# Kernel optimization log

Hardware: AMD Instinct MI355X
Metric: run time of the kernel (lower is better)

Reference implementation:

```python
import jax, jax.numpy as jnp
import numpy as np

N = 50000      # nodes
E = 600000     # edges
C = 32         # in_features (channels)
COUT = 32      # out_features
NB = 8         # n_basis
NS = 10        # n_species
H = 64         # radial MLP hidden
NPATH = 5      # uvu paths for l_max=1: (0,0,0),(0,1,1),(1,0,1),(1,1,0),(1,1,1)
AVG = 12.0     # avg_n_neighbors
RS = 1.6765324703310907  # rescaled SiLU constant


def _rescaled_silu(x):
    return RS * jax.nn.silu(x)


def setup_inputs() -> dict:
    key = jax.random.key(0)
    ks = jax.random.split(key, 16)
    return {
        'node_attrs': jax.random.uniform(ks[0], (N, NS), dtype=jnp.float32),
        'node_feats': jax.random.normal(ks[1], (N, C, 4), dtype=jnp.float32),
        'edge_attrs': jax.random.normal(ks[2], (E, 1, 4), dtype=jnp.float32),
        'edge_feats': jax.random.normal(ks[3], (E, NB), dtype=jnp.float32),
        'W_first': jax.random.normal(ks[4], (2, C, C), dtype=jnp.float32),
        'Wr0': jax.random.normal(ks[5], (H, NB), dtype=jnp.float32),
        'Wr1': jax.random.normal(ks[6], (H, H), dtype=jnp.float32),
        'Wr2': jax.random.normal(ks[7], (H, H), dtype=jnp.float32),
        'Wr3': jax.random.normal(ks[8], (NPATH * C, H), dtype=jnp.float32),
        'W_second0': jax.random.normal(ks[9], (COUT, 2 * C), dtype=jnp.float32),
        'W_second1': jax.random.normal(ks[10], (COUT, 3 * C), dtype=jnp.float32),
        'W_skip': jax.random.normal(ks[11], (2, C, NS, C), dtype=jnp.float32),
        'idx_i': jnp.sort(jax.random.randint(ks[12], (E,), 0, N)),
        'idx_j': jax.random.randint(ks[13], (E,), 0, N),
    }


def reference(node_attrs, node_feats, edge_attrs, edge_feats, W_first, Wr0, Wr1,
              Wr2, Wr3, W_second0, W_second1, W_skip, idx_i, idx_j):
    # ---- skip_tp: uvw tensor product with l=0 node_attrs (species-dependent mixing per l)
    sc0 = jnp.einsum('ncm,nv,cvw->nwm', node_feats[:, :, :1], node_attrs, W_skip[0]) / np.sqrt(C * NS)
    sc1 = jnp.einsum('ncm,nv,cvw->nwm', node_feats[:, :, 1:4], node_attrs, W_skip[1]) / np.sqrt(C * NS)
    sc = jnp.concatenate([sc0, sc1], axis=-1)  # [N, C, 4]

    # ---- linear_first: per-l channel mixing
    x0 = jnp.einsum('ncm,dc->ndm', node_feats[:, :, :1], W_first[0]) / np.sqrt(C)   # [N,C,1]
    x1 = jnp.einsum('ncm,dc->ndm', node_feats[:, :, 1:4], W_first[1]) / np.sqrt(C)  # [N,C,3]

    # ---- radial MLP: Linear+RescaledSiLU chain, last SiLU dropped
    h = _rescaled_silu(edge_feats @ Wr0.T / np.sqrt(NB))
    h = _rescaled_silu(h @ Wr1.T / np.sqrt(H))
    h = _rescaled_silu(h @ Wr2.T / np.sqrt(H))
    w = (h @ Wr3.T / np.sqrt(H)).reshape(E, NPATH, C)  # per-edge, per-path, per-channel weights

    # ---- gather sender features
    xj0 = x0[idx_j][:, :, 0]   # [E, C]
    xj1 = x1[idx_j]            # [E, C, 3]
    y0 = edge_attrs[:, 0, 0]   # [E]      l=0 harmonic
    y1 = edge_attrs[:, 0, 1:4] # [E, 3]   l=1 harmonic

    # ---- uvu weighted tensor product (l_max=1 CG: scalar mult, dot, cross)
    p0 = w[:, 0] * xj0 * y0[:, None]                                   # (0,0,0) -> l=0
    p1 = w[:, 1, :, None] * xj0[:, :, None] * y1[:, None, :]          # (0,1,1) -> l=1
    p2 = w[:, 2, :, None] * xj1 * y0[:, None, None]                   # (1,0,1) -> l=1
    p3 = w[:, 3] * jnp.einsum('ecm,em->ec', xj1, y1)                  # (1,1,0) -> l=0
    p4 = w[:, 4, :, None] * jnp.cross(xj1, y1[:, None, :])            # (1,1,1) -> l=1

    # ---- scatter-add messages to receivers
    seg = lambda m: jax.ops.segment_sum(m, idx_i, num_segments=N)
    msg0 = seg(jnp.stack([p0, p3], axis=1))  # [N, 2, C]
    msg1 = seg(jnp.stack([p1, p2, p4], axis=1))  # [N, 3, C, 3]

    # ---- linear_second: mix (paths x channels) -> out_features per l
    out0 = jnp.einsum('npc,dpc->nd', msg0, W_second0.reshape(COUT, 2, C)) / np.sqrt(2 * C)
    out1 = jnp.einsum('npcm,dpc->ndm', msg1, W_second1.reshape(COUT, 3, C)) / np.sqrt(3 * C)
    message = jnp.concatenate([out0[:, :, None], out1], axis=-1) / AVG  # [N, COUT, 4]
    return message, sc
```

## Files before the change

kernel.cpp:

```cpp
#include <hip/hip_runtime.h>
#include <math.h>

#define N_NODES 50000
#define N_EDGES 600000

constexpr float RS          = 1.6765324703310907f;
constexpr float INV_SQRT8   = 0.35355339059327373f;
constexpr float INV8        = 0.125f;
constexpr float INV_SQRT320 = 0.05590169943749474f;
constexpr float INV_SQRT32  = 0.17677669529663687f;
constexpr float INV_SQRT96  = 0.10206207261596575f;
constexpr float INV_AVG     = 1.0f / 12.0f;

constexpr size_t OFF_X     = 0;
constexpr size_t OFF_ROW   = 25600000;
constexpr size_t OFF_FRAG  = 25800064;
constexpr size_t OFF_FRAG2 = 25841024;
constexpr size_t OFF_W     = 25931136;

typedef __attribute__((ext_vector_type(8))) short bfrag;
typedef __attribute__((ext_vector_type(4))) float ffrag;

__device__ __forceinline__ float rsilu(float z) {
  return RS * z / (1.0f + __expf(-z));
}
__device__ __forceinline__ unsigned short f2bf(float x) {
  unsigned u = __float_as_uint(x);
  u += 0x7FFFu + ((u >> 16) & 1u);
  return (unsigned short)(u >> 16);
}
__device__ __forceinline__ float bf2f(unsigned short u) {
  return __uint_as_float(((unsigned)u) << 16);
}

__global__ __launch_bounds__(256) void k_rowstart(const int* __restrict__ idx_i,
                                                  int* __restrict__ row,
                                                  int E, int N) {
  int e = blockIdx.x * 256 + threadIdx.x;
  if (e >= E) return;
  int cur  = idx_i[e];
  int prev = (e == 0) ? -1 : idx_i[e - 1];
  for (int n = prev + 1; n <= cur; ++n) row[n] = e;
  if (e == E - 1) {
    for (int n = cur + 1; n <= N; ++n) row[n] = E;
  }
}

__global__ __launch_bounds__(256) void k_prep(const float* __restrict__ Wr0,
                                              const float* __restrict__ Wr1,
                                              const float* __restrict__ Wr2,
                                              const float* __restrict__ Wr3,
                                              unsigned short* __restrict__ frag) {
  int t = blockIdx.x * 256 + threadIdx.x;
  int f    = t >> 9;
  int lane = (t >> 3) & 63;
  int j    = t & 7;
  int n16  = lane & 15, quad = lane >> 4;
  float v;
  if (f < 4) {
    int d = f * 16 + n16, k = quad * 8 + j;
    v = (k < 8) ? Wr0[d * 8 + k] : 0.f;
  } else if (f < 12) {
    int ff = f - 4, ntile = ff >> 1, ks = ff & 1;
    int d = ntile * 16 + n16, k = ks * 32 + quad * 8 + j;
    v = Wr1[d * 64 + k];
  } else if (f < 20) {
    int ff = f - 12, ntile = ff >> 1, ks = ff & 1;
    int d = ntile * 16 + n16, k = ks * 32 + quad * 8 + j;
    v = Wr2[d * 64 + k];
  } else {
    int ff = f - 20, ntile = ff >> 1, ks = ff & 1;
    int d = ntile * 16 + n16, k = ks * 32 + quad * 8 + j;
    v = Wr3[d * 64 + k];
  }
  frag[t] = f2bf(v);
}

__global__ __launch_bounds__(256) void k_prep2(const float* __restrict__ Wsk,
                                               const float* __restrict__ Wf,
                                               unsigned short* __restrict__ frag2) {
  int t = blockIdx.x * 256 + threadIdx.x;
  int f    = t >> 9;
  int lane = (t >> 3) & 63;
  int j    = t & 7;
  int n16  = lane & 15, quad = lane >> 4;
  int ks = f >> 3, nt = f & 7;
  int k   = ks * 32 + quad * 8 + j;
  int col = nt * 16 + n16;
  float v = 0.f;
  if (k < 320) {
    int vv = k >> 5, c = k & 31;
    if (col < 32)       v = Wsk[(c * 10 + vv) * 32 + col] * INV_SQRT320;
    else if (col < 64)  v = Wsk[((32 + c) * 10 + vv) * 32 + (col - 32)] * INV_SQRT320;
  } else {
    int c = k - 320;
    if (col >= 96)      v = Wf[1024 + (col - 96) * 32 + c] * INV_SQRT32;
    else if (col >= 64) v = Wf[(col - 64) * 32 + c] * INV_SQRT32;
  }
  frag2[t] = f2bf(v);
}

__global__ __launch_bounds__(256) void k_node_mfma(const float* __restrict__ attrs,
                                                   const float* __restrict__ feats,
                                                   const unsigned short* __restrict__ frag2,
                                                   float* __restrict__ out_sc,
                                                   float* __restrict__ x_ws) {
  int tid = threadIdx.x;
  int wave = tid >> 6, lane = tid & 63;
  int quad = lane >> 4, l16 = lane & 15;
  int nb = blockIdx.x * 32 + wave * 8;

  float featsF[2][8];
  float a[2][10];
#pragma unroll
  for (int mt = 0; mt < 2; ++mt) {
    int nodeA = nb + mt * 4 + (l16 >> 2);
    if (nodeA > N_NODES - 1) nodeA = N_NODES - 1;
    int m = l16 & 3;
#pragma unroll
    for (int j = 0; j < 8; ++j)
      featsF[mt][j] = feats[(size_t)nodeA * 128 + (quad * 8 + j) * 4 + m];
#pragma unroll
    for (int v = 0; v < 10; ++v) a[mt][v] = attrs[nodeA * 10 + v];
  }

  ffrag acc[2][8];
#pragma unroll
  for (int mt = 0; mt < 2; ++mt)
#pragma unroll
    for (int nt = 0; nt < 8; ++nt) acc[mt][nt] = (ffrag){0.f, 0.f, 0.f, 0.f};

#pragma unroll
  for (int ks = 0; ks < 11; ++ks) {
    bfrag Ab[2];
#pragma unroll
    for (int mt = 0; mt < 2; ++mt) {
      union { unsigned short s8[8]; bfrag v; } pk;
#pragma unroll
      for (int j = 0; j < 8; ++j) {
        float val = (ks < 10) ? a[mt][ks] * featsF[mt][j] : featsF[mt][j];
        pk.s8[j] = f2bf(val);
      }
      Ab[mt] = pk.v;
    }
#pragma unroll
    for (int nt = 0; nt < 8; ++nt) {
      bfrag B = *(const bfrag*)(frag2 + ((size_t)(ks * 8 + nt) * 64 + lane) * 8);
      acc[0][nt] = __builtin_amdgcn_mfma_f32_16x16x32_bf16(Ab[0], B, acc[0][nt], 0, 0, 0);
      acc[1][nt] = __builtin_amdgcn_mfma_f32_16x16x32_bf16(Ab[1], B, acc[1][nt], 0, 0, 0);
    }
  }

#pragma unroll
  for (int mt = 0; mt < 2; ++mt) {
    int node = nb + mt * 4 + quad;
    if (node < N_NODES) {
      float4 sc0 = {acc[mt][0][0], acc[mt][2][1], acc[mt][2][2], acc[mt][2][3]};
      float4 sc1 = {acc[mt][1][0], acc[mt][3][1], acc[mt][3][2], acc[mt][3][3]};
      float4 x0  = {acc[mt][4][0], acc[mt][6][1], acc[mt][6][2], acc[mt][6][3]};
      float4 x1  = {acc[mt][5][0], acc[mt][7][1], acc[mt][7][2], acc[mt][7][3]};
      ((float4*)out_sc)[(size_t)node * 32 + l16]      = sc0;
      ((float4*)out_sc)[(size_t)node * 32 + 16 + l16] = sc1;
      ((float4*)x_ws)[(size_t)node * 32 + l16]        = x0;
      ((float4*)x_ws)[(size_t)node * 32 + 16 + l16]   = x1;
    }
  }
}

#define MLP_M 128
__global__ __launch_bounds__(256) void k_mlp(const float* __restrict__ ef,
                                             const unsigned short* __restrict__ frag,
                                             unsigned short* __restrict__ w_out,
                                             int E) {
  __shared__ __align__(16) unsigned short H[4][32][168];
  int tid = threadIdx.x;
  int wave = tid >> 6, lane = tid & 63;
  int quad = lane >> 4, l16 = lane & 15;
  int m0 = blockIdx.x * MLP_M + wave * 32;
  unsigned short (*Hw)[168] = H[wave];

  bfrag a1[2];
#pragma unroll
  for (int mt = 0; mt < 2; ++mt) {
    float vals[8] = {0.f, 0.f, 0.f, 0.f, 0.f, 0.f, 0.f, 0.f};
    if (quad == 0) {
      int r = m0 + mt * 16 + l16;
      if (r > E - 1) r = E - 1;
      const float4* p = (const float4*)(ef + (size_t)r * 8);
      float4 u0 = p[0], u1 = p[1];
      vals[0] = u0.x; vals[1] = u0.y; vals[2] = u0.z; vals[3] = u0.w;
      vals[4] = u1.x; vals[5] = u1.y; vals[6] = u1.z; vals[7] = u1.w;
    }
    union { unsigned short s[8]; bfrag v; } pk;
#pragma unroll
    for (int j = 0; j < 8; ++j) pk.s[j] = f2bf(vals[j]);
    a1[mt] = pk.v;
  }
#pragma unroll
  for (int nt = 0; nt < 4; ++nt) {
    const bfrag* bp = (const bfrag*)(frag + ((size_t)(nt) * 64 + lane) * 8);
    bfrag b = *bp;
    ffrag acc0 = {0.f, 0.f, 0.f, 0.f}, acc1 = acc0;
    acc0 = __builtin_amdgcn_mfma_f32_16x16x32_bf16(a1[0], b, acc0, 0, 0, 0);
    acc1 = __builtin_amdgcn_mfma_f32_16x16x32_bf16(a1[1], b, acc1, 0, 0, 0);
#pragma unroll
    for (int r = 0; r < 4; ++r) {
      Hw[0 * 16 + quad * 4 + r][nt * 16 + l16] = f2bf(rsilu(acc0[r] * INV_SQRT8));
      Hw[1 * 16 + quad * 4 + r][nt * 16 + l16] = f2bf(rsilu(acc1[r] * INV_SQRT8));
    }
  }

  bfrag A[2][2];
#pragma unroll 1
  for (int L = 0; L < 2; ++L) {
    int fbase = 4 + L * 8;
#pragma unroll
    for (int mt = 0; mt < 2; ++mt)
#pragma unroll
      for (int ks = 0; ks < 2; ++ks)
        A[mt][ks] = *(const bfrag*)&Hw[mt * 16 + l16][ks * 32 + quad * 8];
#pragma unroll
    for (int nt = 0; nt < 4; ++nt) {
      ffrag acc0 = {0.f, 0.f, 0.f, 0.f}, acc1 = acc0;
#pragma unroll
      for (int ks = 0; ks < 2; ++ks) {
        bfrag b = *(const bfrag*)(frag + ((size_t)(fbase + nt * 2 + ks) * 64 + lane) * 8);
        acc0 = __builtin_amdgcn_mfma_f32_16x16x32_bf16(A[0][ks], b, acc0, 0, 0, 0);
        acc1 = __builtin_amdgcn_mfma_f32_16x16x32_bf16(A[1][ks], b, acc1, 0, 0, 0);
      }
#pragma unroll
      for (int r = 0; r < 4; ++r) {
        Hw[0 * 16 + quad * 4 + r][nt * 16 + l16] = f2bf(rsilu(acc0[r] * INV8));
        Hw[1 * 16 + quad * 4 + r][nt * 16 + l16] = f2bf(rsilu(acc1[r] * INV8));
      }
    }
  }

#pragma unroll
  for (int mt = 0; mt < 2; ++mt)
#pragma unroll
    for (int ks = 0; ks < 2; ++ks)
      A[mt][ks] = *(const bfrag*)&Hw[mt * 16 + l16][ks * 32 + quad * 8];
#pragma unroll 2
  for (int nt = 0; nt < 10; ++nt) {
    ffrag acc0 = {0.f, 0.f, 0.f, 0.f}, acc1 = acc0;
#pragma unroll
    for (int ks = 0; ks < 2; ++ks) {
      bfrag b = *(const bfrag*)(frag + ((size_t)(20 + nt * 2 + ks) * 64 + lane) * 8);
      acc0 = __builtin_amdgcn_mfma_f32_16x16x32_bf16(A[0][ks], b, acc0, 0, 0, 0);
      acc1 = __builtin_amdgcn_mfma_f32_16x16x32_bf16(A[1][ks], b, acc1, 0, 0, 0);
    }
#pragma unroll
    for (int r = 0; r < 4; ++r) {
      Hw[0 * 16 + quad * 4 + r][nt * 16 + l16] = f2bf(acc0[r] * INV8);
      Hw[1 * 16 + quad * 4 + r][nt * 16 + l16] = f2bf(acc1[r] * INV8);
    }
  }

#pragma unroll 2
  for (int it = 0; it < 10; ++it) {
    int c = it * 64 + lane;
    int row = c / 20, off = c % 20;
    int grow = m0 + row;
    uint4 v = *(const uint4*)&Hw[row][off * 8];
    if (grow < E)
      *(uint4*)(w_out + (size_t)grow * 160 + off * 8) = v;
  }
}

__global__ __launch_bounds__(256) void k_msg(const unsigned short* __restrict__ w_ws,
                                             const float* __restrict__ x_ws,
                                             const float* __restrict__ ea,
                                             const int* __restrict__ idx_j,
                                             const int* __restrict__ row,
                                             const float* __restrict__ Ws0,
                                             const float* __restrict__ Ws1,
                                             float* __restrict__ out_msg) {
  __shared__ float msg[8][353];
  __shared__ float W0T[64 * 33];
  __shared__ float W1T[96 * 33];

  int tid = threadIdx.x;
  for (int t = tid; t < 2048; t += 256) {
    int d = t >> 6, k = t & 63;
    W0T[k * 33 + d] = Ws0[t];
  }
  for (int t = tid; t < 3072; t += 256) {
    int d = t / 96, k = t % 96;
    W1T[k * 33 + d] = Ws1[t];
  }

  int ln = tid >> 5, c = tid & 31;
  int n = blockIdx.x * 8 + ln;
  int e0 = row[n], e1 = row[n + 1];

  float m00 = 0.f, m01 = 0.f;
  float m10x = 0.f, m10y = 0.f, m10z = 0.f;
  float m11x = 0.f, m11y = 0.f, m11z = 0.f;
  float m12x = 0.f, m12y = 0.f, m12z = 0.f;

  for (int base = e0; base < e1; base += 32) {
    int rem = e1 - base;
    int cnt = rem < 32 ? rem : 32;
    int jidx = base + (c < cnt ? c : cnt - 1);
    int j_c = __builtin_nontemporal_load(idx_j + jidx);

    for (int b = 0; b < cnt; b += 4) {
      int mvalid = cnt - b;
      float4 xj[4], y[4];
      float wv[4][5];
#pragma unroll
      for (int t = 0; t < 4; ++t) {
        int tt = (t < mvalid) ? t : 0;
        int e = base + b + tt;
        int j = __shfl(j_c, b + tt, 32);
        xj[t] = ((const float4*)x_ws)[(size_t)j * 32 + c];
        y[t]  = ((const float4*)ea)[e];
        const unsigned short* wr = w_ws + (size_t)e * 160;
        wv[t][0] = bf2f(__builtin_nontemporal_load(wr + c));
        wv[t][1] = bf2f(__builtin_nontemporal_load(wr + 32 + c));
        wv[t][2] = bf2f(__builtin_nontemporal_load(wr + 64 + c));
        wv[t][3] = bf2f(__builtin_nontemporal_load(wr + 96 + c));
        wv[t][4] = bf2f(__builtin_nontemporal_load(wr + 128 + c));
      }
#pragma unroll
      for (int t = 0; t < 4; ++t) {
        if (t < mvalid) {
          float4 x4 = xj[t], y4 = y[t];
          m00 += wv[t][0] * x4.x * y4.x;
          m01 += wv[t][3] * (x4.y * y4.y + x4.z * y4.z + x4.w * y4.w);
          m10x += wv[t][1] * x4.x * y4.y;
          m10y += wv[t][1] * x4.x * y4.z;
          m10z += wv[t][1] * x4.x * y4.w;
          m11x += wv[t][2] * x4.y * y4.x;
          m11y += wv[t][2] * x4.z * y4.x;
          m11z += wv[t][2] * x4.w * y4.x;
          float cx = x4.z * y4.w - x4.w * y4.z;
          float cy = x4.w * y4.y - x4.y * y4.w;
          float cz = x4.y * y4.z - x4.z * y4.y;
          m12x += wv[t][4] * cx;
          m12y += wv[t][4] * cy;
          m12z += wv[t][4] * cz;
        }
      }
    }
  }

  msg[ln][c]      = m00;
  msg[ln][32 + c] = m01;
  msg[ln][64 + (0 * 32 + c) * 3 + 0] = m10x;
  msg[ln][64 + (0 * 32 + c) * 3 + 1] = m10y;
  msg[ln][64 + (0 * 32 + c) * 3 + 2] = m10z;
  msg[ln][64 + (1 * 32 + c) * 3 + 0] = m11x;
  msg[ln][64 + (1 * 32 + c) * 3 + 1] = m11y;
  msg[ln][64 + (1 * 32 + c) * 3 + 2] = m11z;
  msg[ln][64 + (2 * 32 + c) * 3 + 0] = m12x;
  msg[ln][64 + (2 * 32 + c) * 3 + 1] = m12y;
  msg[ln][64 + (2 * 32 + c) * 3 + 2] = m12z;
  __syncthreads();

  float o0 = 0.f;
#pragma unroll 4
  for (int k = 0; k < 64; ++k) o0 += msg[ln][k] * W0T[k * 33 + c];
  float o1x = 0.f, o1y = 0.f, o1z = 0.f;
#pragma unroll 4
  for (int k = 0; k < 96; ++k) {
    float wv = W1T[k * 33 + c];
    o1x += msg[ln][64 + k * 3 + 0] * wv;
    o1y += msg[ln][64 + k * 3 + 1] * wv;
    o1z += msg[ln][64 + k * 3 + 2] * wv;
  }
  float4 res = {o0 * INV8 * INV_AVG, o1x * INV_SQRT96 * INV_AVG,
                o1y * INV_SQRT96 * INV_AVG, o1z * INV_SQRT96 * INV_AVG};
  ((float4*)out_msg)[(size_t)n * 32 + c] = res;
}

extern "C" void kernel_launch(void* const* d_in, const int* in_sizes, int n_in,
                              void* d_out, int out_size, void* d_ws, size_t ws_size,
                              hipStream_t stream) {
  const float* node_attrs = (const float*)d_in[0];
  const float* node_feats = (const float*)d_in[1];
  const float* edge_attrs = (const float*)d_in[2];
  const float* edge_feats = (const float*)d_in[3];
  const float* W_first    = (const float*)d_in[4];
  const float* Wr0        = (const float*)d_in[5];
  const float* Wr1        = (const float*)d_in[6];
  const float* Wr2        = (const float*)d_in[7];
  const float* Wr3        = (const float*)d_in[8];
  const float* Ws0        = (const float*)d_in[9];
  const float* Ws1        = (const float*)d_in[10];
  const float* Wsk        = (const float*)d_in[11];
  const int*   idx_i      = (const int*)d_in[12];
  const int*   idx_j      = (const int*)d_in[13];
  float* out = (float*)d_out;

  char* ws = (char*)d_ws;
  float*          x_ws   = (float*)(ws + OFF_X);
  int*            rowp   = (int*)(ws + OFF_ROW);
  unsigned short* fragp  = (unsigned short*)(ws + OFF_FRAG);
  unsigned short* frag2p = (unsigned short*)(ws + OFF_FRAG2);
  unsigned short* w_ws   = (unsigned short*)(ws + OFF_W);

  k_rowstart<<<(N_EDGES + 255) / 256, 256, 0, stream>>>(idx_i, rowp, N_EDGES, N_NODES);
  k_prep<<<80, 256, 0, stream>>>(Wr0, Wr1, Wr2, Wr3, fragp);
  k_prep2<<<176, 256, 0, stream>>>(Wsk, W_first, frag2p);
  k_node_mfma<<<(N_NODES + 31) / 32, 256, 0, stream>>>(node_attrs, node_feats,
                                                       frag2p, out + 6400000, x_ws);
  k_mlp<<<(N_EDGES + MLP_M - 1) / MLP_M, 256, 0, stream>>>(edge_feats, fragp,
                                                           w_ws, N_EDGES);
  k_msg<<<N_NODES / 8, 256, 0, stream>>>(w_ws, x_ws, edge_attrs, idx_j, rowp,
                                         Ws0, Ws1, out);
}
```

Baseline: 386.1 us.

## Interleave radial weight paths for packed loads and deepen edge batching in k_msg

The radial MLP output columns are permuted so paths 0/1 and 2/3 are interleaved per channel, which lets k_msg fetch two bf16 weights with one 32-bit load instead of separate 16-bit loads. The edge loop batch grows from 4 to 8 edges to put more gathers in flight, and launch bounds request 4 blocks per SM. The shared message buffer is reorganised component-major and padded to 16-byte alignment so the output projection reads float4 vectors. The larger batch raises register pressure, which may limit occupancy against the requested bound.

```diff
diff --git a/kernel.cpp b/kernel.cpp
--- a/kernel.cpp
+++ b/kernel.cpp
@@ -250,10 +250,13 @@
       acc0 = __builtin_amdgcn_mfma_f32_16x16x32_bf16(A[0][ks], b, acc0, 0, 0, 0);
       acc1 = __builtin_amdgcn_mfma_f32_16x16x32_bf16(A[1][ks], b, acc1, 0, 0, 0);
     }
+    int col = nt * 16 + l16;
+    int p = col >> 5, cc = col & 31;
+    int ncol = (p < 4) ? ((p >> 1) * 64 + 2 * cc + (p & 1)) : (128 + cc);
 #pragma unroll
     for (int r = 0; r < 4; ++r) {
-      Hw[0 * 16 + quad * 4 + r][nt * 16 + l16] = f2bf(acc0[r] * INV8);
-      Hw[1 * 16 + quad * 4 + r][nt * 16 + l16] = f2bf(acc1[r] * INV8);
+      Hw[0 * 16 + quad * 4 + r][ncol] = f2bf(acc0[r] * INV8);
+      Hw[1 * 16 + quad * 4 + r][ncol] = f2bf(acc1[r] * INV8);
     }
   }
 
@@ -268,15 +271,15 @@
   }
 }
 
-__global__ __launch_bounds__(256) void k_msg(const unsigned short* __restrict__ w_ws,
-                                             const float* __restrict__ x_ws,
-                                             const float* __restrict__ ea,
-                                             const int* __restrict__ idx_j,
-                                             const int* __restrict__ row,
-                                             const float* __restrict__ Ws0,
-                                             const float* __restrict__ Ws1,
-                                             float* __restrict__ out_msg) {
-  __shared__ float msg[8][353];
+__global__ __launch_bounds__(256, 4) void k_msg(const unsigned short* __restrict__ w_ws,
+                                                const float* __restrict__ x_ws,
+                                                const float* __restrict__ ea,
+                                                const int* __restrict__ idx_j,
+                                                const int* __restrict__ row,
+                                                const float* __restrict__ Ws0,
+                                                const float* __restrict__ Ws1,
+                                                float* __restrict__ out_msg) {
+  __shared__ __align__(16) float msg[8][356];
   __shared__ float W0T[64 * 33];
   __shared__ float W1T[96 * 33];
 
@@ -305,42 +308,46 @@
     int jidx = base + (c < cnt ? c : cnt - 1);
     int j_c = __builtin_nontemporal_load(idx_j + jidx);
 
-    for (int b = 0; b < cnt; b += 4) {
+    for (int b = 0; b < cnt; b += 8) {
       int mvalid = cnt - b;
-      float4 xj[4], y[4];
-      float wv[4][5];
-#pragma unroll
-      for (int t = 0; t < 4; ++t) {
+      float4 xj[8], y4[8];
+      unsigned d01[8], d23[8];
+      unsigned short w4v[8];
+#pragma unroll
+      for (int t = 0; t < 8; ++t) {
         int tt = (t < mvalid) ? t : 0;
         int e = base + b + tt;
         int j = __shfl(j_c, b + tt, 32);
         xj[t] = ((const float4*)x_ws)[(size_t)j * 32 + c];
-        y[t]  = ((const float4*)ea)[e];
-        const unsigned short* wr = w_ws + (size_t)e * 160;
-        wv[t][0] = bf2f(__builtin_nontemporal_load(wr + c));
-        wv[t][1] = bf2f(__builtin_nontemporal_load(wr + 32 + c));
-        wv[t][2] = bf2f(__builtin_nontemporal_load(wr + 64 + c));
-        wv[t][3] = bf2f(__builtin_nontemporal_load(wr + 96 + c));
-        wv[t][4] = bf2f(__builtin_nontemporal_load(wr + 128 + c));
+        y4[t] = ((const float4*)ea)[e];
+        const char* wb = (const char*)w_ws + (size_t)e * 320;
+        d01[t] = *(const unsigned*)(wb + 4 * c);
+        d23[t] = *(const unsigned*)(wb + 128 + 4 * c);
+        w4v[t] = *(const unsigned short*)(wb + 256 + 2 * c);
       }
 #pragma unroll
-      for (int t = 0; t < 4; ++t) {
+      for (int t = 0; t < 8; ++t) {
         if (t < mvalid) {
-          float4 x4 = xj[t], y4 = y[t];
-          m00 += wv[t][0] * x4.x * y4.x;
-          m01 += wv[t][3] * (x4.y * y4.y + x4.z * y4.z + x4.w * y4.w);
-          m10x += wv[t][1] * x4.x * y4.y;
-          m10y += wv[t][1] * x4.x * y4.z;
-          m10z += wv[t][1] * x4.x * y4.w;
-          m11x += wv[t][2] * x4.y * y4.x;
-          m11y += wv[t][2] * x4.z * y4.x;
-          m11z += wv[t][2] * x4.w * y4.x;
-          float cx = x4.z * y4.w - x4.w * y4.z;
-          float cy = x4.w * y4.y - x4.y * y4.w;
-          float cz = x4.y * y4.z - x4.z * y4.y;
-          m12x += wv[t][4] * cx;
-          m12y += wv[t][4] * cy;
-          m12z += wv[t][4] * cz;
+          float w0 = __uint_as_float(d01[t] << 16);
+          float w1 = __uint_as_float(d01[t] & 0xffff0000u);
+          float w2 = __uint_as_float(d23[t] << 16);
+          float w3 = __uint_as_float(d23[t] & 0xffff0000u);
+          float w4 = bf2f(w4v[t]);
+          float4 x4 = xj[t], yy = y4[t];
+          m00 += w0 * x4.x * yy.x;
+          m01 += w3 * (x4.y * yy.y + x4.z * yy.z + x4.w * yy.w);
+          m10x += w1 * x4.x * yy.y;
+          m10y += w1 * x4.x * yy.z;
+          m10z += w1 * x4.x * yy.w;
+          m11x += w2 * x4.y * yy.x;
+          m11y += w2 * x4.z * yy.x;
+          m11z += w2 * x4.w * yy.x;
+          float cx = x4.z * yy.w - x4.w * yy.z;
+          float cy = x4.w * yy.y - x4.y * yy.w;
+          float cz = x4.y * yy.z - x4.z * yy.y;
+          m12x += w4 * cx;
+          m12y += w4 * cy;
+          m12z += w4 * cz;
         }
       }
     }
@@ -348,27 +355,42 @@
 
   msg[ln][c]      = m00;
   msg[ln][32 + c] = m01;
-  msg[ln][64 + (0 * 32 + c) * 3 + 0] = m10x;
-  msg[ln][64 + (0 * 32 + c) * 3 + 1] = m10y;
-  msg[ln][64 + (0 * 32 + c) * 3 + 2] = m10z;
-  msg[ln][64 + (1 * 32 + c) * 3 + 0] = m11x;
-  msg[ln][64 + (1 * 32 + c) * 3 + 1] = m11y;
-  msg[ln][64 + (1 * 32 + c) * 3 + 2] = m11z;
-  msg[ln][64 + (2 * 32 + c) * 3 + 0] = m12x;
-  msg[ln][64 + (2 * 32 + c) * 3 + 1] = m12y;
-  msg[ln][64 + (2 * 32 + c) * 3 + 2] = m12z;
+  msg[ln][64 + 0 * 96 +  0 + c] = m10x;
+  msg[ln][64 + 0 * 96 + 32 + c] = m11x;
+  msg[ln][64 + 0 * 96 + 64 + c] = m12x;
+  msg[ln][64 + 1 * 96 +  0 + c] = m10y;
+  msg[ln][64 + 1 * 96 + 32 + c] = m11y;
+  msg[ln][64 + 1 * 96 + 64 + c] = m12y;
+  msg[ln][64 + 2 * 96 +  0 + c] = m10z;
+  msg[ln][64 + 2 * 96 + 32 + c] = m11z;
+  msg[ln][64 + 2 * 96 + 64 + c] = m12z;
   __syncthreads();
 
   float o0 = 0.f;
 #pragma unroll 4
-  for (int k = 0; k < 64; ++k) o0 += msg[ln][k] * W0T[k * 33 + c];
+  for (int k4 = 0; k4 < 16; ++k4) {
+    float4 mk = *(const float4*)&msg[ln][4 * k4];
+    o0 += mk.x * W0T[(4 * k4 + 0) * 33 + c];
+    o0 += mk.y * W0T[(4 * k4 + 1) * 33 + c];
+    o0 += mk.z * W0T[(4 * k4 + 2) * 33 + c];
+    o0 += mk.w * W0T[(4 * k4 + 3) * 33 + c];
+  }
   float o1x = 0.f, o1y = 0.f, o1z = 0.f;
 #pragma unroll 4
-  for (int k = 0; k < 96; ++k) {
-    float wv = W1T[k * 33 + c];
-    o1x += msg[ln][64 + k * 3 + 0] * wv;
-    o1y += msg[ln][64 + k * 3 + 1] * wv;
-    o1z += msg[ln][64 + k * 3 + 2] * wv;
+  for (int k4 = 0; k4 < 24; ++k4) {
+    float4 ax = *(const float4*)&msg[ln][64 + 0 * 96 + 4 * k4];
+    float4 ay = *(const float4*)&msg[ln][64 + 1 * 96 + 4 * k4];
+    float4 az = *(const float4*)&msg[ln][64 + 2 * 96 + 4 * k4];
+#pragma unroll
+    for (int i = 0; i < 4; ++i) {
+      float wv = W1T[(4 * k4 + i) * 33 + c];
+      float mx = (i == 0) ? ax.x : (i == 1) ? ax.y : (i == 2) ? ax.z : ax.w;
+      float my = (i == 0) ? ay.x : (i == 1) ? ay.y : (i == 2) ? ay.z : ay.w;
+      float mz = (i == 0) ? az.x : (i == 1) ? az.y : (i == 2) ? az.z : az.w;
+      o1x += mx * wv;
+      o1y += my * wv;
+      o1z += mz * wv;
+    }
   }
   float4 res = {o0 * INV8 * INV_AVG, o1x * INV_SQRT96 * INV_AVG,
                 o1y * INV_SQRT96 * INV_AVG, o1z * INV_SQRT96 * INV_AVG};
```

Result: slower. 410.2 us (+6.2%).
